# Kernel tuning notes

Measured on AMD Instinct MI355X. Metric: run time of the kernel, lower is better.

Reference implementation:

```python
import jax, jax.numpy as jnp
import numpy as np

B, C, H, W = 16, 512, 64, 64

def _conv1x1_relu(x, Wk, bk):
    # 1x1 conv (stride 1) + ReLU, as in the conv2d helper
    return jax.nn.relu(jnp.einsum('bchw,oc->bohw', x, Wk) + bk[None, :, None, None])

def _maxpool2(t):
    b, c, h, w = t.shape
    return t.reshape(b, c, h // 2, 2, w // 2, 2).max(axis=(3, 5))

def setup_inputs() -> dict:
    key = jax.random.key(0)
    ks = jax.random.split(key, 10)
    s = 0.05
    x = jax.random.normal(ks[0], (B, C, H, W), jnp.float32)
    W_theta = jax.random.normal(ks[1], (C // 8, C), jnp.float32) * s
    b_theta = jnp.zeros((C // 8,), jnp.float32)
    W_phi = jax.random.normal(ks[2], (C // 8, C), jnp.float32) * s
    b_phi = jnp.zeros((C // 8,), jnp.float32)
    W_g = jax.random.normal(ks[3], (C // 2, C), jnp.float32) * s
    b_g = jnp.zeros((C // 2,), jnp.float32)
    W_o = jax.random.normal(ks[4], (C, C // 2), jnp.float32) * s
    b_o = jnp.zeros((C,), jnp.float32)
    gamma = jnp.array([0.5], jnp.float32)  # nonzero so attention branch contributes
    return {"x": x, "W_theta": W_theta, "b_theta": b_theta, "W_phi": W_phi,
            "b_phi": b_phi, "W_g": W_g, "b_g": b_g, "W_o": W_o, "b_o": b_o,
            "gamma": gamma}

def reference(x, W_theta, b_theta, W_phi, b_phi, W_g, b_g, W_o, b_o, gamma):
    theta = _conv1x1_relu(x, W_theta, b_theta).reshape(B, C // 8, H * W)
    phi = _maxpool2(_conv1x1_relu(x, W_phi, b_phi)).reshape(B, C // 8, H * W // 4)
    g = _maxpool2(_conv1x1_relu(x, W_g, b_g)).reshape(B, C // 2, H * W // 4)
    # beta[b, n, m] = softmax_m(theta^T phi)
    beta = jax.nn.softmax(jnp.einsum('bcn,bcm->bnm', theta, phi), axis=-1)
    # o[b, c, n] = g @ beta^T
    o = jnp.einsum('bcm,bnm->bcn', g, beta).reshape(B, C // 2, H, W)
    o = _conv1x1_relu(o, W_o, b_o)
    return gamma[0] * o + x
```

## Files before the change

kernel.cpp:

```cpp
#include <hip/hip_runtime.h>
#include <cstdint>
#include <cstddef>

#define BB 16
#define CIN 512
#define NPIX 4096
#define C8 64
#define C2 256
#define MM 1024

using bf16x8 = __attribute__((ext_vector_type(8))) short;
using f32x4  = __attribute__((ext_vector_type(4))) float;

__device__ __forceinline__ short f2bf(float f) {
  union { float f; unsigned u; } v; v.f = f;
  unsigned r = v.u + 0x7FFFu + ((v.u >> 16) & 1u);
  return (short)(r >> 16);
}
__device__ __forceinline__ unsigned cvtpk(float lo, float hi) {
  unsigned r;
  asm("v_cvt_pk_bf16_f32 %0, %1, %2" : "=v"(r) : "v"(lo), "v"(hi));
  return r;
}
__device__ __forceinline__ bf16x8 ldg8(const short* p) {
  return *reinterpret_cast<const bf16x8*>(p);
}
__device__ __forceinline__ bf16x8 lds8(const short* p) {
  union { unsigned long long q[2]; bf16x8 v; } u;
  u.q[0] = *reinterpret_cast<const unsigned long long*>(p);
  u.q[1] = *reinterpret_cast<const unsigned long long*>(p + 4);
  return u.v;
}
__device__ __forceinline__ void sts8(short* p, bf16x8 v) {
  union { unsigned long long q[2]; bf16x8 v; } u; u.v = v;
  *reinterpret_cast<unsigned long long*>(p) = u.q[0];
  *reinterpret_cast<unsigned long long*>(p + 4) = u.q[1];
}
#define MFMA(a, b, c) __builtin_amdgcn_mfma_f32_16x16x32_bf16(a, b, c, 0, 0, 0)
#define LOG2E 1.4426950408889634f

__global__ __launch_bounds__(256) void cast_w_k(const float* __restrict__ wa,
                                                const float* __restrict__ wb,
                                                const float* __restrict__ wc,
                                                const float* __restrict__ wd,
                                                short* __restrict__ out) {
  int i = blockIdx.x * 256 + threadIdx.x;
  float v;
  if (i < 32768) v = wa[i] * LOG2E;
  else if (i < 65536) v = wb[i - 32768];
  else if (i < 196608) v = wc[i - 65536];
  else v = wd[i - 196608];
  out[i] = f2bf(v);
}

__global__ __launch_bounds__(1024) void conv_mega_k(
    const float* __restrict__ x, const short* __restrict__ wbf,
    const float* __restrict__ bth, const float* __restrict__ bph,
    const float* __restrict__ bg,
    short* __restrict__ thetaT, short* __restrict__ phiT,
    short* __restrict__ gp) {
  __shared__ __align__(16) short xs[128][36];
  const int t = threadIdx.x, w = t >> 6, l = t & 63;
  const int lr = l & 15, quad = l >> 4;
  const int wg = w & 7, wh = w >> 3;
  const int bx = blockIdx.x, b = blockIdx.y;
  const int nbase = bx * 128;
  const float* xb = x + ((size_t)b * CIN << 12) + nbase;

  const int nl = t & 127, cg = t >> 7;

  f32x4 acc[3][4];
#pragma unroll
  for (int i = 0; i < 3; ++i)
#pragma unroll
    for (int j = 0; j < 4; ++j) acc[i][j] = (f32x4){0.f, 0.f, 0.f, 0.f};

  float pv0[2][2], pv1[2][2];
#pragma unroll
  for (int s = 0; s < 2; ++s)
#pragma unroll
    for (int p = 0; p < 2; ++p) {
      int cl = s * 32 + (p * 8 + cg) * 2;
      pv0[s][p] = xb[((size_t)cl << 12) + nl];
      pv1[s][p] = xb[((size_t)(cl + 1) << 12) + nl];
    }

  for (int c0 = 0; c0 < CIN; c0 += 32) {
    const int slot = (c0 >> 5) & 1;
    bf16x8 af[3];
#pragma unroll
    for (int tt = 0; tt < 3; ++tt)
      af[tt] = ldg8(wbf + (size_t)(wg * 48 + tt * 16 + lr) * CIN + c0 + quad * 8);
    asm volatile("s_waitcnt lgkmcnt(0)" ::: "memory");
    __builtin_amdgcn_s_barrier();
#pragma unroll
    for (int p = 0; p < 2; ++p) {
      int cl = (p * 8 + cg) * 2;
      *reinterpret_cast<unsigned*>(&xs[nl][cl]) = cvtpk(pv0[slot][p], pv1[slot][p]);
    }
    asm volatile("s_waitcnt lgkmcnt(0)" ::: "memory");
    __builtin_amdgcn_s_barrier();
    if (c0 + 64 < CIN) {
#pragma unroll
      for (int p = 0; p < 2; ++p) {
        int cl = (p * 8 + cg) * 2;
        pv0[slot][p] = xb[((size_t)(c0 + 64 + cl) << 12) + nl];
        pv1[slot][p] = xb[((size_t)(c0 + 64 + cl + 1) << 12) + nl];
      }
    }
    __builtin_amdgcn_s_setprio(1);
#pragma unroll
    for (int j = 0; j < 4; ++j) {
      const int gnt = (j & 1) + wh * 2 + (j >> 1) * 4;
      bf16x8 bfr = lds8(&xs[gnt * 16 + lr][quad * 8]);
#pragma unroll
      for (int tt = 0; tt < 3; ++tt)
        acc[tt][j] = MFMA(af[tt], bfr, acc[tt][j]);
    }
    __builtin_amdgcn_s_setprio(0);
  }

#pragma unroll
  for (int tt = 0; tt < 3; ++tt) {
    const int ocb = wg * 48 + tt * 16;
    if (ocb < 64) {
      short* tb = thetaT + ((size_t)b << 12) * C8;
#pragma unroll
      for (int r = 0; r < 4; ++r) {
        int oc = ocb + quad * 4 + r;
        float bia = bth[oc] * LOG2E;
#pragma unroll
        for (int j = 0; j < 4; ++j) {
          const int gnt = (j & 1) + wh * 2 + (j >> 1) * 4;
          int n = nbase + gnt * 16 + lr;
          tb[(size_t)n * C8 + oc] = f2bf(fmaxf(acc[tt][j][r] + bia, 0.f));
        }
      }
    } else if (ocb < 128) {
      short* pb = phiT + ((size_t)b << 10) * C8;
#pragma unroll
      for (int r = 0; r < 4; ++r) {
        int oc = ocb - 64 + quad * 4 + r;
        float bia = bph[oc];
#pragma unroll
        for (int jj = 0; jj < 2; ++jj) {
          float va = fmaxf(acc[tt][jj][r] + bia, 0.f);
          float vb = fmaxf(acc[tt][jj + 2][r] + bia, 0.f);
          float pa = fmaxf(va, __shfl_xor(va, 1));
          float pbv = fmaxf(vb, __shfl_xor(vb, 1));
          float pool = fmaxf(pa, pbv);
          if ((l & 1) == 0) {
            int m = bx * 32 + wh * 16 + jj * 8 + (lr >> 1);
            pb[(size_t)m * C8 + oc] = f2bf(pool);
          }
        }
      }
    } else {
      short* gb = gp + ((size_t)b << 10) * C2;
#pragma unroll
      for (int r = 0; r < 4; ++r) {
        int oc = ocb - 128 + quad * 4 + r;
        float bia = bg[oc];
#pragma unroll
        for (int jj = 0; jj < 2; ++jj) {
          float va = fmaxf(acc[tt][jj][r] + bia, 0.f);
          float vb = fmaxf(acc[tt][jj + 2][r] + bia, 0.f);
          float pa = fmaxf(va, __shfl_xor(va, 1));
          float pbv = fmaxf(vb, __shfl_xor(vb, 1));
          float pool = fmaxf(pa, pbv);
          if ((l & 1) == 0) {
            int m = bx * 32 + wh * 16 + jj * 8 + (lr >> 1);
            gb[(size_t)oc * MM + m] = f2bf(pool);
          }
        }
      }
    }
  }
}

__global__ __launch_bounds__(256, 2) void attn_k(
    const short* __restrict__ thetaT, const short* __restrict__ phiT,
    const short* __restrict__ gp, const short* __restrict__ wo,
    const float* __restrict__ bo, const float* __restrict__ x,
    const float* __restrict__ gamma, float* __restrict__ out) {
  __shared__ __align__(16) short smem[16896];
  __shared__ __align__(16) short phs[128][68];
  __shared__ float balpha[2][4][16];
  __shared__ float binv[4][16];
  const int t = threadIdx.x, w = t >> 6, l = t & 63;
  const int lr = l & 15, quad = l >> 4;
  const int blk = blockIdx.x;
  const int b = ((blk & 7) << 1) | ((blk >> 3) & 1);
  const int q0 = (blk >> 4) << 6;
  const int nw = q0 + w * 16;

  const short* thb = thetaT + ((size_t)b << 12) * C8;
  const short* phb = phiT + ((size_t)b << 10) * C8;
  const short* gpb = gp + ((size_t)b << 10) * C2;

  bf16x8 tb0 = ldg8(thb + (size_t)(nw + lr) * C8 + quad * 8);
  bf16x8 tb1 = ldg8(thb + (size_t)(nw + lr) * C8 + 32 + quad * 8);

  f32x4 oacc[4][4];
#pragma unroll
  for (int i = 0; i < 4; ++i)
#pragma unroll
    for (int j = 0; j < 4; ++j) oacc[i][j] = (f32x4){0.f, 0.f, 0.f, 0.f};
  float mrun = -3e38f, ssum = 0.f;

  const int srow = t >> 3, scol = (t & 7) * 8;
  bf16x8 stld[4];
  auto stage_phi_issue = [&](int ch) {
    const int m0 = ch * 128;
#pragma unroll
    for (int sw = 0; sw < 4; ++sw)
      stld[sw] = ldg8(phb + (size_t)(m0 + sw * 32 + srow) * C8 + scol);
  };
  auto stage_phi_write = [&]() {
#pragma unroll
    for (int sw = 0; sw < 4; ++sw)
      sts8(&phs[sw * 32 + srow][scol], stld[sw]);
  };

  auto scores = [&](int ch) {
    const int buf = ch & 1;
    f32x4 sacc[8];
#pragma unroll
    for (int i = 0; i < 8; ++i) sacc[i] = (f32x4){0.f, 0.f, 0.f, 0.f};
    __builtin_amdgcn_s_setprio(1);
#pragma unroll
    for (int mt = 0; mt < 8; ++mt) {
      const short* pr = &phs[mt * 16 + lr][quad * 8];
      sacc[mt] = MFMA(lds8(pr), tb0, sacc[mt]);
      sacc[mt] = MFMA(lds8(pr + 32), tb1, sacc[mt]);
    }
    __builtin_amdgcn_s_setprio(0);
    float cmax = sacc[0][0];
#pragma unroll
    for (int mt = 0; mt < 8; ++mt)
      cmax = fmaxf(cmax, fmaxf(fmaxf(sacc[mt][0], sacc[mt][1]),
                               fmaxf(sacc[mt][2], sacc[mt][3])));
    cmax = fmaxf(cmax, __shfl_xor(cmax, 16));
    cmax = fmaxf(cmax, __shfl_xor(cmax, 32));
    const float mnew = (cmax > mrun + 8.f) ? cmax : mrun;
    const float al = exp2f(mrun - mnew);
    mrun = mnew;
    float rsum = 0.f;
    short* prow = smem + ((((buf << 2) | w) << 4) + lr) * 132;
#pragma unroll
    for (int mt = 0; mt < 8; ++mt) {
      float e0 = exp2f(sacc[mt][0] - mnew);
      float e1 = exp2f(sacc[mt][1] - mnew);
      float e2 = exp2f(sacc[mt][2] - mnew);
      float e3 = exp2f(sacc[mt][3] - mnew);
      rsum += (e0 + e1) + (e2 + e3);
      uint2 pk2;
      pk2.x = cvtpk(e0, e1);
      pk2.y = cvtpk(e2, e3);
      *reinterpret_cast<uint2*>(prow + mt * 16 + quad * 4) = pk2;
    }
    ssum = ssum * al + rsum;
    if (quad == 0) balpha[buf][w][lr] = al;
  };

  bf16x8 gpf[16];
  auto pfga = [&](int ch) {
    const int m0 = ch * 128;
#pragma unroll
    for (int kc = 0; kc < 4; ++kc)
#pragma unroll
      for (int ct = 0; ct < 4; ++ct)
        gpf[kc * 4 + ct] = ldg8(gpb + (size_t)(w * 64 + ct * 16 + lr) * MM +
                                m0 + kc * 32 + quad * 8);
  };

  stage_phi_issue(0);
  stage_phi_write();
  asm volatile("s_waitcnt lgkmcnt(0)" ::: "memory");
  __builtin_amdgcn_s_barrier();
  scores(0);
  pfga(0);

  for (int ch = 0; ch < 8; ++ch) {
    const int buf = ch & 1;
    asm volatile("s_waitcnt lgkmcnt(0)" ::: "memory");
    __builtin_amdgcn_s_barrier();
    if (ch < 7) stage_phi_issue(ch + 1);
    float av[4];
#pragma unroll
    for (int qt = 0; qt < 4; ++qt) av[qt] = balpha[buf][qt][lr];
    if (av[0] != 1.f || av[1] != 1.f || av[2] != 1.f || av[3] != 1.f) {
#pragma unroll
      for (int ct = 0; ct < 4; ++ct)
#pragma unroll
        for (int qt = 0; qt < 4; ++qt) oacc[ct][qt] *= av[qt];
    }
    __builtin_amdgcn_s_setprio(1);
#pragma unroll
    for (int kc = 0; kc < 4; ++kc) {
      bf16x8 pf[4];
#pragma unroll
      for (int qt = 0; qt < 4; ++qt)
        pf[qt] = lds8(smem + ((((buf << 2) | qt) << 4) + lr) * 132 +
                      kc * 32 + quad * 8);
#pragma unroll
      for (int ct = 0; ct < 4; ++ct)
#pragma unroll
        for (int qt = 0; qt < 4; ++qt)
          oacc[ct][qt] = MFMA(gpf[kc * 4 + ct], pf[qt], oacc[ct][qt]);
    }
    __builtin_amdgcn_s_setprio(0);
    if (ch < 7) {
      stage_phi_write();
      asm volatile("s_waitcnt lgkmcnt(0)" ::: "memory");
      __builtin_amdgcn_s_barrier();
      scores(ch + 1);
      pfga(ch + 1);
    }
  }

  ssum += __shfl_xor(ssum, 16);
  ssum += __shfl_xor(ssum, 32);
  if (quad == 0) binv[w][lr] = 1.f / ssum;
  __syncthreads();
  float invn[4];
#pragma unroll
  for (int qt = 0; qt < 4; ++qt) invn[qt] = binv[qt][lr];

  short (*os)[264] = reinterpret_cast<short (*)[264]>(smem);
#pragma unroll
  for (int ct = 0; ct < 4; ++ct) {
    int c0 = w * 64 + ct * 16 + quad * 4;
#pragma unroll
    for (int qt = 0; qt < 4; ++qt) {
      uint2 pk2;
      pk2.x = cvtpk(oacc[ct][qt][0] * invn[qt], oacc[ct][qt][1] * invn[qt]);
      pk2.y = cvtpk(oacc[ct][qt][2] * invn[qt], oacc[ct][qt][3] * invn[qt]);
      *reinterpret_cast<uint2*>(&os[qt * 16 + lr][c0]) = pk2;
    }
  }
  __syncthreads();

  const float g0 = gamma[0];
  for (int pp = 0; pp < 4; ++pp) {
    const int ocb = w * 128 + pp * 32;
    f32x4 acc2[2][4];
#pragma unroll
    for (int i = 0; i < 2; ++i)
#pragma unroll
      for (int j = 0; j < 4; ++j) acc2[i][j] = (f32x4){0.f, 0.f, 0.f, 0.f};
#pragma unroll
    for (int half = 0; half < 2; ++half) {
      bf16x8 wa[8];
#pragma unroll
      for (int k2 = 0; k2 < 4; ++k2)
#pragma unroll
        for (int ot = 0; ot < 2; ++ot)
          wa[k2 * 2 + ot] = ldg8(wo + (size_t)(ocb + ot * 16 + lr) * C2 +
                                 (half * 4 + k2) * 32 + quad * 8);
      __builtin_amdgcn_s_setprio(1);
#pragma unroll
      for (int k2 = 0; k2 < 4; ++k2) {
        const int kc = half * 4 + k2;
        bf16x8 of[4];
#pragma unroll
        for (int qt = 0; qt < 4; ++qt)
          of[qt] = lds8(&os[qt * 16 + lr][kc * 32 + quad * 8]);
#pragma unroll
        for (int ot = 0; ot < 2; ++ot)
#pragma unroll
          for (int qt = 0; qt < 4; ++qt)
            acc2[ot][qt] = MFMA(wa[k2 * 2 + ot], of[qt], acc2[ot][qt]);
      }
      __builtin_amdgcn_s_setprio(0);
    }
#pragma unroll
    for (int ot = 0; ot < 2; ++ot) {
#pragma unroll
      for (int r = 0; r < 4; ++r) {
        int oc = ocb + ot * 16 + quad * 4 + r;
        float bia = bo[oc];
        size_t base = ((size_t)(b * CIN + oc) << 12);
#pragma unroll
        for (int qt = 0; qt < 4; ++qt) {
          int n = q0 + qt * 16 + lr;
          float v = g0 * fmaxf(acc2[ot][qt][r] + bia, 0.f);
          out[base + n] = v + x[base + n];
        }
      }
    }
  }
}

extern "C" void kernel_launch(void* const* d_in, const int* in_sizes, int n_in,
                              void* d_out, int out_size, void* d_ws, size_t ws_size,
                              hipStream_t stream) {
  const float* x       = (const float*)d_in[0];
  const float* W_theta = (const float*)d_in[1];
  const float* b_theta = (const float*)d_in[2];
  const float* W_phi   = (const float*)d_in[3];
  const float* b_phi   = (const float*)d_in[4];
  const float* W_g     = (const float*)d_in[5];
  const float* b_g     = (const float*)d_in[6];
  const float* W_o     = (const float*)d_in[7];
  const float* b_o     = (const float*)d_in[8];
  const float* gamma   = (const float*)d_in[9];
  float* out = (float*)d_out;
  char* W = (char*)d_ws;

  short* thetaT = (short*)(W);
  short* phiT   = (short*)(W + 8388608);
  short* gp     = (short*)(W + 10485760);
  short* wbf    = (short*)(W + 18874368);
  short* wo     = wbf + 196608;

  cast_w_k<<<dim3(1280), 256, 0, stream>>>(W_theta, W_phi, W_g, W_o, wbf);
  conv_mega_k<<<dim3(32, 16), 1024, 0, stream>>>(x, wbf, b_theta, b_phi, b_g,
                                                 thetaT, phiT, gp);
  attn_k<<<dim3(1024), 256, 0, stream>>>(thetaT, phiT, gp, wo, b_o, x, gamma, out);
}
```

Measured before the change: 401.1 us.

## Halve attention query tile per block, split key range across waves, raise occupancy

The attention kernel now processes 32 queries per block instead of 64, doubling the grid to 2048 blocks. Wave pairs split each 128-key chunk and combine row maxima and sums through shared memory with an extra barrier. The g-operand prefetch array shrinks from 16 to 4 registers and is streamed per k-chunk, and launch bounds rise to 4 blocks per CU. The aim is fewer VGPRs and less LDS per block, so more waves can hide memory latency. In exchange, phi and W_o are reloaded by twice as many blocks, there are more barriers, and the g loads sit on the MFMA critical path.

```diff
diff --git a/kernel.cpp b/kernel.cpp
--- a/kernel.cpp
+++ b/kernel.cpp
@@ -178,34 +178,36 @@
   }
 }
 
-__global__ __launch_bounds__(256, 2) void attn_k(
+__global__ __launch_bounds__(256, 4) void attn_k(
     const short* __restrict__ thetaT, const short* __restrict__ phiT,
     const short* __restrict__ gp, const short* __restrict__ wo,
     const float* __restrict__ bo, const float* __restrict__ x,
     const float* __restrict__ gamma, float* __restrict__ out) {
-  __shared__ __align__(16) short smem[16896];
+  __shared__ __align__(16) short smem[8448];
   __shared__ __align__(16) short phs[128][68];
-  __shared__ float balpha[2][4][16];
-  __shared__ float binv[4][16];
+  __shared__ float cm[4][16];
+  __shared__ float balpha[2][2][16];
+  __shared__ float bsum[4][16];
+  __shared__ float binv[2][16];
   const int t = threadIdx.x, w = t >> 6, l = t & 63;
   const int lr = l & 15, quad = l >> 4;
+  const int qh = w & 1, mh = w >> 1;
   const int blk = blockIdx.x;
   const int b = ((blk & 7) << 1) | ((blk >> 3) & 1);
-  const int q0 = (blk >> 4) << 6;
-  const int nw = q0 + w * 16;
+  const int q0 = (blk >> 4) << 5;
 
   const short* thb = thetaT + ((size_t)b << 12) * C8;
   const short* phb = phiT + ((size_t)b << 10) * C8;
   const short* gpb = gp + ((size_t)b << 10) * C2;
 
-  bf16x8 tb0 = ldg8(thb + (size_t)(nw + lr) * C8 + quad * 8);
-  bf16x8 tb1 = ldg8(thb + (size_t)(nw + lr) * C8 + 32 + quad * 8);
-
-  f32x4 oacc[4][4];
+  bf16x8 tb0 = ldg8(thb + (size_t)(q0 + qh * 16 + lr) * C8 + quad * 8);
+  bf16x8 tb1 = ldg8(thb + (size_t)(q0 + qh * 16 + lr) * C8 + 32 + quad * 8);
+
+  f32x4 oacc[4][2];
 #pragma unroll
   for (int i = 0; i < 4; ++i)
 #pragma unroll
-    for (int j = 0; j < 4; ++j) oacc[i][j] = (f32x4){0.f, 0.f, 0.f, 0.f};
+    for (int j = 0; j < 2; ++j) oacc[i][j] = (f32x4){0.f, 0.f, 0.f, 0.f};
   float mrun = -3e38f, ssum = 0.f;
 
   const int srow = t >> 3, scol = (t & 7) * 8;
@@ -224,31 +226,35 @@
 
   auto scores = [&](int ch) {
     const int buf = ch & 1;
-    f32x4 sacc[8];
-#pragma unroll
-    for (int i = 0; i < 8; ++i) sacc[i] = (f32x4){0.f, 0.f, 0.f, 0.f};
+    f32x4 sacc[4];
+#pragma unroll
+    for (int i = 0; i < 4; ++i) sacc[i] = (f32x4){0.f, 0.f, 0.f, 0.f};
     __builtin_amdgcn_s_setprio(1);
 #pragma unroll
-    for (int mt = 0; mt < 8; ++mt) {
-      const short* pr = &phs[mt * 16 + lr][quad * 8];
+    for (int mt = 0; mt < 4; ++mt) {
+      const short* pr = &phs[mh * 64 + mt * 16 + lr][quad * 8];
       sacc[mt] = MFMA(lds8(pr), tb0, sacc[mt]);
       sacc[mt] = MFMA(lds8(pr + 32), tb1, sacc[mt]);
     }
     __builtin_amdgcn_s_setprio(0);
     float cmax = sacc[0][0];
 #pragma unroll
-    for (int mt = 0; mt < 8; ++mt)
+    for (int mt = 0; mt < 4; ++mt)
       cmax = fmaxf(cmax, fmaxf(fmaxf(sacc[mt][0], sacc[mt][1]),
                                fmaxf(sacc[mt][2], sacc[mt][3])));
     cmax = fmaxf(cmax, __shfl_xor(cmax, 16));
     cmax = fmaxf(cmax, __shfl_xor(cmax, 32));
-    const float mnew = (cmax > mrun + 8.f) ? cmax : mrun;
+    if (quad == 0) cm[w][lr] = cmax;
+    asm volatile("s_waitcnt lgkmcnt(0)" ::: "memory");
+    __builtin_amdgcn_s_barrier();
+    const float cboth = fmaxf(cmax, cm[w ^ 2][lr]);
+    const float mnew = (cboth > mrun + 8.f) ? cboth : mrun;
     const float al = exp2f(mrun - mnew);
     mrun = mnew;
     float rsum = 0.f;
-    short* prow = smem + ((((buf << 2) | w) << 4) + lr) * 132;
-#pragma unroll
-    for (int mt = 0; mt < 8; ++mt) {
+    short* prow = smem + ((buf * 32 + qh * 16 + lr) * 132) + mh * 64;
+#pragma unroll
+    for (int mt = 0; mt < 4; ++mt) {
       float e0 = exp2f(sacc[mt][0] - mnew);
       float e1 = exp2f(sacc[mt][1] - mnew);
       float e2 = exp2f(sacc[mt][2] - mnew);
@@ -260,18 +266,15 @@
       *reinterpret_cast<uint2*>(prow + mt * 16 + quad * 4) = pk2;
     }
     ssum = ssum * al + rsum;
-    if (quad == 0) balpha[buf][w][lr] = al;
+    if (quad == 0 && mh == 0) balpha[buf][qh][lr] = al;
   };
 
-  bf16x8 gpf[16];
+  bf16x8 gpf[4];
   auto pfga = [&](int ch) {
     const int m0 = ch * 128;
 #pragma unroll
-    for (int kc = 0; kc < 4; ++kc)
-#pragma unroll
-      for (int ct = 0; ct < 4; ++ct)
-        gpf[kc * 4 + ct] = ldg8(gpb + (size_t)(w * 64 + ct * 16 + lr) * MM +
-                                m0 + kc * 32 + quad * 8);
+    for (int ct = 0; ct < 4; ++ct)
+      gpf[ct] = ldg8(gpb + (size_t)(w * 64 + ct * 16 + lr) * MM + m0 + quad * 8);
   };
 
   stage_phi_issue(0);
@@ -282,32 +285,45 @@
   pfga(0);
 
   for (int ch = 0; ch < 8; ++ch) {
-    const int buf = ch & 1;
+    const int buf = ch & 1, m0 = ch * 128;
     asm volatile("s_waitcnt lgkmcnt(0)" ::: "memory");
     __builtin_amdgcn_s_barrier();
     if (ch < 7) stage_phi_issue(ch + 1);
-    float av[4];
-#pragma unroll
-    for (int qt = 0; qt < 4; ++qt) av[qt] = balpha[buf][qt][lr];
-    if (av[0] != 1.f || av[1] != 1.f || av[2] != 1.f || av[3] != 1.f) {
+    float av0 = balpha[buf][0][lr], av1 = balpha[buf][1][lr];
+    if (av0 != 1.f || av1 != 1.f) {
+#pragma unroll
+      for (int ct = 0; ct < 4; ++ct) {
+        oacc[ct][0] *= av0;
+        oacc[ct][1] *= av1;
+      }
+    }
+    __builtin_amdgcn_s_setprio(1);
+    bf16x8 cga[4];
+#pragma unroll
+    for (int ct = 0; ct < 4; ++ct) cga[ct] = gpf[ct];
+#pragma unroll
+    for (int kc = 0; kc < 4; ++kc) {
+      bf16x8 nga[4];
+      if (kc < 3) {
+#pragma unroll
+        for (int ct = 0; ct < 4; ++ct)
+          nga[ct] = ldg8(gpb + (size_t)(w * 64 + ct * 16 + lr) * MM +
+                         m0 + (kc + 1) * 32 + quad * 8);
+      }
+      bf16x8 pf[2];
+#pragma unroll
+      for (int qt = 0; qt < 2; ++qt)
+        pf[qt] = lds8(smem + ((buf * 32 + qt * 16 + lr) * 132) +
+                      kc * 32 + quad * 8);
 #pragma unroll
       for (int ct = 0; ct < 4; ++ct)
 #pragma unroll
-        for (int qt = 0; qt < 4; ++qt) oacc[ct][qt] *= av[qt];
-    }
-    __builtin_amdgcn_s_setprio(1);
-#pragma unroll
-    for (int kc = 0; kc < 4; ++kc) {
-      bf16x8 pf[4];
-#pragma unroll
-      for (int qt = 0; qt < 4; ++qt)
-        pf[qt] = lds8(smem + ((((buf << 2) | qt) << 4) + lr) * 132 +
-                      kc * 32 + quad * 8);
-#pragma unroll
-      for (int ct = 0; ct < 4; ++ct)
-#pragma unroll
-        for (int qt = 0; qt < 4; ++qt)
-          oacc[ct][qt] = MFMA(gpf[kc * 4 + ct], pf[qt], oacc[ct][qt]);
+        for (int qt = 0; qt < 2; ++qt)
+          oacc[ct][qt] = MFMA(cga[ct], pf[qt], oacc[ct][qt]);
+      if (kc < 3) {
+#pragma unroll
+        for (int i = 0; i < 4; ++i) cga[i] = nga[i];
+      }
     }
     __builtin_amdgcn_s_setprio(0);
     if (ch < 7) {
@@ -321,18 +337,18 @@
 
   ssum += __shfl_xor(ssum, 16);
   ssum += __shfl_xor(ssum, 32);
-  if (quad == 0) binv[w][lr] = 1.f / ssum;
+  if (quad == 0) bsum[w][lr] = ssum;
   __syncthreads();
-  float invn[4];
-#pragma unroll
-  for (int qt = 0; qt < 4; ++qt) invn[qt] = binv[qt][lr];
+  if (quad == 0 && mh == 0) binv[qh][lr] = 1.f / (bsum[w][lr] + bsum[w ^ 2][lr]);
+  __syncthreads();
+  float invn[2] = {binv[0][lr], binv[1][lr]};
 
   short (*os)[264] = reinterpret_cast<short (*)[264]>(smem);
 #pragma unroll
   for (int ct = 0; ct < 4; ++ct) {
     int c0 = w * 64 + ct * 16 + quad * 4;
 #pragma unroll
-    for (int qt = 0; qt < 4; ++qt) {
+    for (int qt = 0; qt < 2; ++qt) {
       uint2 pk2;
       pk2.x = cvtpk(oacc[ct][qt][0] * invn[qt], oacc[ct][qt][1] * invn[qt]);
       pk2.y = cvtpk(oacc[ct][qt][2] * invn[qt], oacc[ct][qt][3] * invn[qt]);
@@ -344,11 +360,11 @@
   const float g0 = gamma[0];
   for (int pp = 0; pp < 4; ++pp) {
     const int ocb = w * 128 + pp * 32;
-    f32x4 acc2[2][4];
+    f32x4 acc2[2][2];
 #pragma unroll
     for (int i = 0; i < 2; ++i)
 #pragma unroll
-      for (int j = 0; j < 4; ++j) acc2[i][j] = (f32x4){0.f, 0.f, 0.f, 0.f};
+      for (int j = 0; j < 2; ++j) acc2[i][j] = (f32x4){0.f, 0.f, 0.f, 0.f};
 #pragma unroll
     for (int half = 0; half < 2; ++half) {
       bf16x8 wa[8];
@@ -362,14 +378,14 @@
 #pragma unroll
       for (int k2 = 0; k2 < 4; ++k2) {
         const int kc = half * 4 + k2;
-        bf16x8 of[4];
-#pragma unroll
-        for (int qt = 0; qt < 4; ++qt)
+        bf16x8 of[2];
+#pragma unroll
+        for (int qt = 0; qt < 2; ++qt)
           of[qt] = lds8(&os[qt * 16 + lr][kc * 32 + quad * 8]);
 #pragma unroll
         for (int ot = 0; ot < 2; ++ot)
 #pragma unroll
-          for (int qt = 0; qt < 4; ++qt)
+          for (int qt = 0; qt < 2; ++qt)
             acc2[ot][qt] = MFMA(wa[k2 * 2 + ot], of[qt], acc2[ot][qt]);
       }
       __builtin_amdgcn_s_setprio(0);
@@ -382,7 +398,7 @@
         float bia = bo[oc];
         size_t base = ((size_t)(b * CIN + oc) << 12);
 #pragma unroll
-        for (int qt = 0; qt < 4; ++qt) {
+        for (int qt = 0; qt < 2; ++qt) {
           int n = q0 + qt * 16 + lr;
           float v = g0 * fmaxf(acc2[ot][qt][r] + bia, 0.f);
           out[base + n] = v + x[base + n];
@@ -417,5 +433,5 @@
   cast_w_k<<<dim3(1280), 256, 0, stream>>>(W_theta, W_phi, W_g, W_o, wbf);
   conv_mega_k<<<dim3(32, 16), 1024, 0, stream>>>(x, wbf, b_theta, b_phi, b_g,
                                                  thetaT, phiT, gp);
-  attn_k<<<dim3(1024), 256, 0, stream>>>(thetaT, phiT, gp, wo, b_o, x, gamma, out);
-}
+  attn_k<<<dim3(2048), 256, 0, stream>>>(thetaT, phiT, gp, wo, b_o, x, gamma, out);
+}
```

After: 495.9 us. 23.6% more time.

## Double-buffer conv LDS tile and halve block to 512 threads with 8 n-tiles per wave

Applied to the files above, without the earlier changes.

The fused 1x1 conv kernel now runs 8 waves, each covering all 128 pixels (8 n-tiles) for its 48 output channels, instead of 16 waves splitting pixels. Each wave loads its weight fragments once per k-step instead of twice. The x tile in LDS is double-buffered, so the next slice is converted and stored while the current one feeds the MFMAs, leaving one barrier per iteration instead of two. The cost is more accumulator registers per thread (96 floats) and fewer waves per block to hide latency.

```diff
diff --git a/kernel.cpp b/kernel.cpp
--- a/kernel.cpp
+++ b/kernel.cpp
@@ -53,76 +53,89 @@
   out[i] = f2bf(v);
 }
 
-__global__ __launch_bounds__(1024) void conv_mega_k(
+__global__ __launch_bounds__(512) void conv_mega_k(
     const float* __restrict__ x, const short* __restrict__ wbf,
     const float* __restrict__ bth, const float* __restrict__ bph,
     const float* __restrict__ bg,
     short* __restrict__ thetaT, short* __restrict__ phiT,
     short* __restrict__ gp) {
-  __shared__ __align__(16) short xs[128][36];
+  __shared__ __align__(16) short xs[2][128][36];
   const int t = threadIdx.x, w = t >> 6, l = t & 63;
   const int lr = l & 15, quad = l >> 4;
-  const int wg = w & 7, wh = w >> 3;
   const int bx = blockIdx.x, b = blockIdx.y;
   const int nbase = bx * 128;
   const float* xb = x + ((size_t)b * CIN << 12) + nbase;
 
-  const int nl = t & 127, cg = t >> 7;
-
-  f32x4 acc[3][4];
+  const int nl = t & 127, cp = t >> 7;
+
+  f32x4 acc[3][8];
 #pragma unroll
   for (int i = 0; i < 3; ++i)
 #pragma unroll
-    for (int j = 0; j < 4; ++j) acc[i][j] = (f32x4){0.f, 0.f, 0.f, 0.f};
-
-  float pv0[2][2], pv1[2][2];
+    for (int j = 0; j < 8; ++j) acc[i][j] = (f32x4){0.f, 0.f, 0.f, 0.f};
+
+  float pv0[2][4], pv1[2][4];
 #pragma unroll
   for (int s = 0; s < 2; ++s)
 #pragma unroll
-    for (int p = 0; p < 2; ++p) {
-      int cl = s * 32 + (p * 8 + cg) * 2;
+    for (int p = 0; p < 4; ++p) {
+      int cl = s * 32 + (p * 4 + cp) * 2;
       pv0[s][p] = xb[((size_t)cl << 12) + nl];
       pv1[s][p] = xb[((size_t)(cl + 1) << 12) + nl];
     }
-
-  for (int c0 = 0; c0 < CIN; c0 += 32) {
-    const int slot = (c0 >> 5) & 1;
+#pragma unroll
+  for (int p = 0; p < 4; ++p) {
+    int cl = (p * 4 + cp) * 2;
+    *reinterpret_cast<unsigned*>(&xs[0][nl][cl]) = cvtpk(pv0[0][p], pv1[0][p]);
+  }
+#pragma unroll
+  for (int p = 0; p < 4; ++p) {
+    int cl = 64 + (p * 4 + cp) * 2;
+    pv0[0][p] = xb[((size_t)cl << 12) + nl];
+    pv1[0][p] = xb[((size_t)(cl + 1) << 12) + nl];
+  }
+  asm volatile("s_waitcnt lgkmcnt(0)" ::: "memory");
+  __builtin_amdgcn_s_barrier();
+
+#pragma unroll
+  for (int i = 0; i < 16; ++i) {
+    const int c0 = i * 32, buf = i & 1;
     bf16x8 af[3];
 #pragma unroll
     for (int tt = 0; tt < 3; ++tt)
-      af[tt] = ldg8(wbf + (size_t)(wg * 48 + tt * 16 + lr) * CIN + c0 + quad * 8);
+      af[tt] = ldg8(wbf + (size_t)(w * 48 + tt * 16 + lr) * CIN + c0 + quad * 8);
+    if (i < 15) {
+#pragma unroll
+      for (int p = 0; p < 4; ++p) {
+        int cl = (p * 4 + cp) * 2;
+        *reinterpret_cast<unsigned*>(&xs[buf ^ 1][nl][cl]) =
+            cvtpk(pv0[buf ^ 1][p], pv1[buf ^ 1][p]);
+      }
+      if (i < 13) {
+#pragma unroll
+        for (int p = 0; p < 4; ++p) {
+          int cl = (i + 3) * 32 + (p * 4 + cp) * 2;
+          pv0[buf ^ 1][p] = xb[((size_t)cl << 12) + nl];
+          pv1[buf ^ 1][p] = xb[((size_t)(cl + 1) << 12) + nl];
+        }
+      }
+    }
+    __builtin_amdgcn_s_setprio(1);
+#pragma unroll
+    for (int nt = 0; nt < 8; ++nt) {
+      bf16x8 bfr = lds8(&xs[buf][nt * 16 + lr][quad * 8]);
+#pragma unroll
+      for (int tt = 0; tt < 3; ++tt)
+        acc[tt][nt] = MFMA(af[tt], bfr, acc[tt][nt]);
+    }
+    __builtin_amdgcn_s_setprio(0);
     asm volatile("s_waitcnt lgkmcnt(0)" ::: "memory");
     __builtin_amdgcn_s_barrier();
-#pragma unroll
-    for (int p = 0; p < 2; ++p) {
-      int cl = (p * 8 + cg) * 2;
-      *reinterpret_cast<unsigned*>(&xs[nl][cl]) = cvtpk(pv0[slot][p], pv1[slot][p]);
-    }
-    asm volatile("s_waitcnt lgkmcnt(0)" ::: "memory");
-    __builtin_amdgcn_s_barrier();
-    if (c0 + 64 < CIN) {
-#pragma unroll
-      for (int p = 0; p < 2; ++p) {
-        int cl = (p * 8 + cg) * 2;
-        pv0[slot][p] = xb[((size_t)(c0 + 64 + cl) << 12) + nl];
-        pv1[slot][p] = xb[((size_t)(c0 + 64 + cl + 1) << 12) + nl];
-      }
-    }
-    __builtin_amdgcn_s_setprio(1);
-#pragma unroll
-    for (int j = 0; j < 4; ++j) {
-      const int gnt = (j & 1) + wh * 2 + (j >> 1) * 4;
-      bf16x8 bfr = lds8(&xs[gnt * 16 + lr][quad * 8]);
-#pragma unroll
-      for (int tt = 0; tt < 3; ++tt)
-        acc[tt][j] = MFMA(af[tt], bfr, acc[tt][j]);
-    }
-    __builtin_amdgcn_s_setprio(0);
   }
 
 #pragma unroll
   for (int tt = 0; tt < 3; ++tt) {
-    const int ocb = wg * 48 + tt * 16;
+    const int ocb = w * 48 + tt * 16;
     if (ocb < 64) {
       short* tb = thetaT + ((size_t)b << 12) * C8;
 #pragma unroll
@@ -130,10 +143,9 @@
         int oc = ocb + quad * 4 + r;
         float bia = bth[oc] * LOG2E;
 #pragma unroll
-        for (int j = 0; j < 4; ++j) {
-          const int gnt = (j & 1) + wh * 2 + (j >> 1) * 4;
-          int n = nbase + gnt * 16 + lr;
-          tb[(size_t)n * C8 + oc] = f2bf(fmaxf(acc[tt][j][r] + bia, 0.f));
+        for (int nt = 0; nt < 8; ++nt) {
+          int n = nbase + nt * 16 + lr;
+          tb[(size_t)n * C8 + oc] = f2bf(fmaxf(acc[tt][nt][r] + bia, 0.f));
         }
       }
     } else if (ocb < 128) {
@@ -143,14 +155,14 @@
         int oc = ocb - 64 + quad * 4 + r;
         float bia = bph[oc];
 #pragma unroll
-        for (int jj = 0; jj < 2; ++jj) {
-          float va = fmaxf(acc[tt][jj][r] + bia, 0.f);
-          float vb = fmaxf(acc[tt][jj + 2][r] + bia, 0.f);
+        for (int nt = 0; nt < 4; ++nt) {
+          float va = fmaxf(acc[tt][nt][r] + bia, 0.f);
+          float vb = fmaxf(acc[tt][nt + 4][r] + bia, 0.f);
           float pa = fmaxf(va, __shfl_xor(va, 1));
           float pbv = fmaxf(vb, __shfl_xor(vb, 1));
           float pool = fmaxf(pa, pbv);
           if ((l & 1) == 0) {
-            int m = bx * 32 + wh * 16 + jj * 8 + (lr >> 1);
+            int m = bx * 32 + nt * 8 + (lr >> 1);
             pb[(size_t)m * C8 + oc] = f2bf(pool);
           }
         }
@@ -162,14 +174,14 @@
         int oc = ocb - 128 + quad * 4 + r;
         float bia = bg[oc];
 #pragma unroll
-        for (int jj = 0; jj < 2; ++jj) {
-          float va = fmaxf(acc[tt][jj][r] + bia, 0.f);
-          float vb = fmaxf(acc[tt][jj + 2][r] + bia, 0.f);
+        for (int nt = 0; nt < 4; ++nt) {
+          float va = fmaxf(acc[tt][nt][r] + bia, 0.f);
+          float vb = fmaxf(acc[tt][nt + 4][r] + bia, 0.f);
           float pa = fmaxf(va, __shfl_xor(va, 1));
           float pbv = fmaxf(vb, __shfl_xor(vb, 1));
           float pool = fmaxf(pa, pbv);
           if ((l & 1) == 0) {
-            int m = bx * 32 + wh * 16 + jj * 8 + (lr >> 1);
+            int m = bx * 32 + nt * 8 + (lr >> 1);
             gb[(size_t)oc * MM + m] = f2bf(pool);
           }
         }
@@ -415,7 +427,7 @@
   short* wo     = wbf + 196608;
 
   cast_w_k<<<dim3(1280), 256, 0, stream>>>(W_theta, W_phi, W_g, W_o, wbf);
-  conv_mega_k<<<dim3(32, 16), 1024, 0, stream>>>(x, wbf, b_theta, b_phi, b_g,
-                                                 thetaT, phiT, gp);
+  conv_mega_k<<<dim3(32, 16), 512, 0, stream>>>(x, wbf, b_theta, b_phi, b_g,
+                                                thetaT, phiT, gp);
   attn_k<<<dim3(1024), 256, 0, stream>>>(thetaT, phiT, gp, wo, b_o, x, gamma, out);
 }
```

Result: no change. 393.2 us (-2.0%).
